# Optimization experiments

Measured on AMD Instinct MI355X. Metric: run time of the kernel, lower is better.

Reference implementation:

```python
import jax, jax.numpy as jnp
import numpy as np

EMBED_DIM = 1024
N_HEADS = 16
HEAD_DIM = EMBED_DIM // N_HEADS
N_CATS = 5
SCALE = float(np.sqrt(HEAD_DIM))


def setup_inputs() -> dict:
    key = jax.random.key(0)
    ks = jax.random.split(key, 16)
    B, S = 2, 2048
    inp = {
        "query": jax.random.normal(ks[0], (B, S, EMBED_DIM), jnp.float32),
        "key_": jax.random.normal(ks[1], (B, S, EMBED_DIM), jnp.float32),
        "value": jax.random.normal(ks[2], (B, S, EMBED_DIM), jnp.float32),
        "responses": jax.random.randint(ks[3], (B, S), 0, N_CATS),
        "mask": jnp.ones((B, S, S), jnp.int32),
        # Linear params (torch convention: y = x @ W.T + b)
        "Wq": jax.random.normal(ks[4], (EMBED_DIM, EMBED_DIM), jnp.float32) * 0.02,
        "bq": jnp.zeros((EMBED_DIM,), jnp.float32),
        "Wk": jax.random.normal(ks[5], (EMBED_DIM, EMBED_DIM), jnp.float32) * 0.02,
        "bk": jnp.zeros((EMBED_DIM,), jnp.float32),
        "Wv": jax.random.normal(ks[6], (EMBED_DIM, EMBED_DIM), jnp.float32) * 0.02,
        "bv": jnp.zeros((EMBED_DIM,), jnp.float32),
        "Wo": jax.random.normal(ks[7], (EMBED_DIM, EMBED_DIM), jnp.float32) * 0.02,
        "bo": jnp.zeros((EMBED_DIM,), jnp.float32),
        # qwk_modulation: Linear(1, n_heads)
        "Wm": jax.random.normal(ks[8], (N_HEADS, 1), jnp.float32) * 0.5,
        "bm": jnp.zeros((N_HEADS,), jnp.float32),
    }
    return inp


def _qwk_matrix():
    i = jnp.arange(N_CATS, dtype=jnp.float32)
    return 1.0 - (i[:, None] - i[None, :]) ** 2 / (N_CATS - 1) ** 2  # [C, C]


def reference(query, key_, value, responses, mask,
              Wq, bq, Wk, bk, Wv, bv, Wo, bo, Wm, bm):
    B, S, E = query.shape
    # projections
    Q = (query @ Wq.T + bq).reshape(B, S, N_HEADS, HEAD_DIM).transpose(0, 2, 1, 3)
    K = (key_ @ Wk.T + bk).reshape(B, S, N_HEADS, HEAD_DIM).transpose(0, 2, 1, 3)
    V = (value @ Wv.T + bv).reshape(B, S, N_HEADS, HEAD_DIM).transpose(0, 2, 1, 3)
    scores = jnp.einsum("bhqd,bhkd->bhqk", Q, K) / SCALE  # [B,H,S,S]
    # QWK ordinal bias: gather pairwise weight, tiny linear 1->H, broadcast-add
    qwk = _qwk_matrix()
    pair = qwk[responses[:, :, None], responses[:, None, :]]  # [B,S,S]
    # Linear(1, n_heads): bias[...,None] @ Wm.T + bm -> [B,S,S,H] -> [B,H,S,S]
    head_bias = pair[:, None, :, :] * Wm[:, 0][None, :, None, None] + bm[None, :, None, None]
    scores = scores + head_bias
    scores = jnp.where(mask[:, None, :, :] == 0, -1e9, scores)
    attn = jax.nn.softmax(scores, axis=-1)
    attended = jnp.einsum("bhqk,bhkd->bhqd", attn, V)
    attended = attended.transpose(0, 2, 1, 3).reshape(B, S, E)
    return attended @ Wo.T + bo
```

## Files before the change

### kernel.cpp

```cpp
#include <hip/hip_runtime.h>
#include <hip/hip_bf16.h>
#include <stdint.h>

#define S_LEN 2048
#define EMB   1024
#define NHEAD 16
#define HDIM  64
#define BATCH 2

typedef __bf16 bf16x8 __attribute__((ext_vector_type(8)));
typedef float  f32x4  __attribute__((ext_vector_type(4)));

__device__ __forceinline__ void gll16(const void* g, void* l) {
  __builtin_amdgcn_global_load_lds(
      (const __attribute__((address_space(1))) void*)g,
      (__attribute__((address_space(3))) void*)l,
      16, 0, 0);
}

__global__ void __launch_bounds__(256) cast_mask_kernel(
    const float* __restrict__ s0, const float* __restrict__ s1, const float* __restrict__ s2,
    const float* __restrict__ s3, const float* __restrict__ s4, const float* __restrict__ s5,
    const float* __restrict__ s6,
    __hip_bfloat16* __restrict__ d0, __hip_bfloat16* __restrict__ d1,
    __hip_bfloat16* __restrict__ d2, __hip_bfloat16* __restrict__ d3,
    __hip_bfloat16* __restrict__ d4, __hip_bfloat16* __restrict__ d5,
    __hip_bfloat16* __restrict__ d6,
    const int* __restrict__ mask, unsigned* __restrict__ flags) {
  const int z = blockIdx.y;
  const int t = threadIdx.x;
  if (z == 7) {
    const int kt = blockIdx.x & 15, qt = (blockIdx.x >> 4) & 31, b = (int)blockIdx.x >> 9;
    const int* base = mask + ((size_t)b * S_LEN + (size_t)qt * 64) * S_LEN + (size_t)kt * 128;
    int ok = 1;
#pragma unroll
    for (int p = 0; p < 8; ++p) {
      int idx = p * 256 + t;
      int row = idx >> 5, c4 = idx & 31;
      const int4 v = *(const int4*)(base + (size_t)row * S_LEN + c4 * 4);
      ok &= (v.x != 0) & (v.y != 0) & (v.z != 0) & (v.w != 0);
    }
    unsigned long long bl = __ballot(ok);
    __shared__ unsigned long long bw[4];
    bw[t >> 6] = bl;
    __syncthreads();
    if (t == 0) {
      unsigned all = ((bw[0] & bw[1] & bw[2] & bw[3]) == ~0ull) ? 1u : 0u;
      flags[((size_t)b * 32 + qt) * 16 + kt] = all;
    }
    return;
  }
  const float* s = (z == 0) ? s0 : (z == 1) ? s1 : (z == 2) ? s2 : (z == 3) ? s3
                 : (z == 4) ? s4 : (z == 5) ? s5 : s6;
  __hip_bfloat16* d = (z == 0) ? d0 : (z == 1) ? d1 : (z == 2) ? d2 : (z == 3) ? d3
                    : (z == 4) ? d4 : (z == 5) ? d5 : d6;
  const int n = (z < 3) ? (BATCH * S_LEN * EMB) : (EMB * EMB);
  const size_t i = ((size_t)blockIdx.x * 256 + t) * 16;
  if (i >= (size_t)n) return;
  __hip_bfloat16 tmp[16];
#pragma unroll
  for (int j = 0; j < 4; ++j) {
    const float4 v = *(const float4*)(s + i + j * 4);
    tmp[j * 4 + 0] = __float2bfloat16(v.x);
    tmp[j * 4 + 1] = __float2bfloat16(v.y);
    tmp[j * 4 + 2] = __float2bfloat16(v.z);
    tmp[j * 4 + 3] = __float2bfloat16(v.w);
  }
  *(bf16x8*)(d + i)     = *(bf16x8*)&tmp[0];
  *(bf16x8*)(d + i + 8) = *(bf16x8*)&tmp[8];
}

__global__ void __launch_bounds__(256, 2)
gemm_kernel(const __hip_bfloat16* __restrict__ A0, const __hip_bfloat16* __restrict__ A1,
            const __hip_bfloat16* __restrict__ A2,
            const __hip_bfloat16* __restrict__ W0, const __hip_bfloat16* __restrict__ W1,
            const __hip_bfloat16* __restrict__ W2,
            const float* __restrict__ b0, const float* __restrict__ b1,
            const float* __restrict__ b2,
            __hip_bfloat16* __restrict__ O0, __hip_bfloat16* __restrict__ O1,
            __hip_bfloat16* __restrict__ O2) {
  __shared__ __align__(16) __hip_bfloat16 As[128 * 64];
  __shared__ __align__(16) __hip_bfloat16 Bs[128 * 64];

  const int L = blockIdx.x;
  const int m0 = (L & 31) * 128;
  const int n0 = ((L >> 5) & 7) * 128;
  const int z  = L >> 8;

  const __hip_bfloat16* A  = (z == 0) ? A0 : ((z == 1) ? A1 : A2);
  const __hip_bfloat16* W  = (z == 0) ? W0 : ((z == 1) ? W1 : W2);
  const float* bi          = (z == 0) ? b0 : ((z == 1) ? b1 : b2);
  __hip_bfloat16* O        = (z == 0) ? O0 : ((z == 1) ? O1 : O2);

  const int t = threadIdx.x;
  const int w = t >> 6, lane = t & 63, quad = lane >> 4, l15 = lane & 15;
  const int wr = w >> 1, wc = w & 1;

  f32x4 acc[4][4];
#pragma unroll
  for (int i = 0; i < 4; ++i)
#pragma unroll
    for (int j = 0; j < 4; ++j) acc[i][j] = (f32x4)0.0f;

  const int srow = t >> 3;
  const int scb  = (t & 7) ^ (srow & 7);
  const __hip_bfloat16* Ap = A + (size_t)(m0 + srow) * EMB + (scb << 3);
  const __hip_bfloat16* Wp = W + (size_t)(n0 + srow) * EMB + (scb << 3);

  for (int k0 = 0; k0 < EMB; k0 += 64) {
    __syncthreads();
#pragma unroll
    for (int rnd = 0; rnd < 4; ++rnd) {
      gll16(Ap + (size_t)(rnd * 32) * EMB + k0, &As[(rnd * 256 + (w << 6)) * 8]);
      gll16(Wp + (size_t)(rnd * 32) * EMB + k0, &Bs[(rnd * 256 + (w << 6)) * 8]);
    }
    __syncthreads();

    bf16x8 af[4][2], bfr[4][2];
#pragma unroll
    for (int i = 0; i < 4; ++i) {
      const int ra = wr * 64 + i * 16 + l15;
#pragma unroll
      for (int hh = 0; hh < 2; ++hh)
        af[i][hh] = *(const bf16x8*)&As[ra * 64 + ((((hh << 2) + quad) ^ (l15 & 7)) << 3)];
    }
#pragma unroll
    for (int j = 0; j < 4; ++j) {
      const int rbw = wc * 64 + j * 16 + l15;
#pragma unroll
      for (int hh = 0; hh < 2; ++hh)
        bfr[j][hh] = *(const bf16x8*)&Bs[rbw * 64 + ((((hh << 2) + quad) ^ (l15 & 7)) << 3)];
    }
#pragma unroll
    for (int hh = 0; hh < 2; ++hh)
#pragma unroll
      for (int i = 0; i < 4; ++i)
#pragma unroll
        for (int j = 0; j < 4; ++j)
          acc[i][j] =
              __builtin_amdgcn_mfma_f32_16x16x32_bf16(af[i][hh], bfr[j][hh], acc[i][j], 0, 0, 0);
  }

#pragma unroll
  for (int j = 0; j < 4; ++j) {
    const int ng = n0 + wc * 64 + j * 16 + l15;
    const float bb = bi[ng];
    const int h = ng >> 6, d = ng & 63;
#pragma unroll
    for (int i = 0; i < 4; ++i) {
#pragma unroll
      for (int r = 0; r < 4; ++r) {
        const int mg = m0 + wr * 64 + i * 16 + quad * 4 + r;
        const int b = mg >> 11, s = mg & 2047;
        float v = acc[i][j][r] + bb;
        if (z == 0) {
          O[(((size_t)b * NHEAD + h) * S_LEN + s) * HDIM + d] =
              __float2bfloat16(v * (0.125f * 1.4426950408889634f));
        } else if (z == 1) {
          O[(((size_t)b * NHEAD + h) * S_LEN + s) * HDIM + d] = __float2bfloat16(v);
        } else {
          const size_t idx = (size_t)(b * NHEAD + h) * 131072 + (size_t)(s >> 7) * 8192 +
                             (size_t)((((s >> 5) & 3) * 4 + ((s >> 2) & 3)) * 64 + d) * 8 +
                             ((s >> 4) & 1) * 4 + (s & 3);
          O[idx] = __float2bfloat16(v);
        }
      }
    }
  }
}

__global__ void __launch_bounds__(256, 2)
gemm_o_kernel(const __hip_bfloat16* __restrict__ A, const __hip_bfloat16* __restrict__ W,
              const float* __restrict__ bi, float* __restrict__ O) {
  __shared__ __align__(16) __hip_bfloat16 As[64 * 64];
  __shared__ __align__(16) __hip_bfloat16 Bs[128 * 64];
  const int L = blockIdx.x;
  const int m0 = (L & 63) * 64;
  const int n0 = (L >> 6) * 128;
  const int t = threadIdx.x;
  const int w = t >> 6, lane = t & 63, quad = lane >> 4, l15 = lane & 15;
  const int wr = w >> 1, wc = w & 1;

  f32x4 acc[2][4];
#pragma unroll
  for (int i = 0; i < 2; ++i)
#pragma unroll
    for (int j = 0; j < 4; ++j) acc[i][j] = (f32x4)0.0f;

  const int srow = t >> 3;
  const int scb  = (t & 7) ^ (srow & 7);
  const __hip_bfloat16* Ap = A + (size_t)(m0 + srow) * EMB + (scb << 3);
  const __hip_bfloat16* Wp = W + (size_t)(n0 + srow) * EMB + (scb << 3);

  for (int k0 = 0; k0 < EMB; k0 += 64) {
    __syncthreads();
#pragma unroll
    for (int rnd = 0; rnd < 2; ++rnd)
      gll16(Ap + (size_t)(rnd * 32) * EMB + k0, &As[(rnd * 256 + (w << 6)) * 8]);
#pragma unroll
    for (int rnd = 0; rnd < 4; ++rnd)
      gll16(Wp + (size_t)(rnd * 32) * EMB + k0, &Bs[(rnd * 256 + (w << 6)) * 8]);
    __syncthreads();

    bf16x8 af[2][2], bfr[4][2];
#pragma unroll
    for (int i = 0; i < 2; ++i) {
      const int ra = wr * 32 + i * 16 + l15;
#pragma unroll
      for (int hh = 0; hh < 2; ++hh)
        af[i][hh] = *(const bf16x8*)&As[ra * 64 + ((((hh << 2) + quad) ^ (l15 & 7)) << 3)];
    }
#pragma unroll
    for (int j = 0; j < 4; ++j) {
      const int rbw = wc * 64 + j * 16 + l15;
#pragma unroll
      for (int hh = 0; hh < 2; ++hh)
        bfr[j][hh] = *(const bf16x8*)&Bs[rbw * 64 + ((((hh << 2) + quad) ^ (l15 & 7)) << 3)];
    }
#pragma unroll
    for (int hh = 0; hh < 2; ++hh)
#pragma unroll
      for (int i = 0; i < 2; ++i)
#pragma unroll
        for (int j = 0; j < 4; ++j)
          acc[i][j] =
              __builtin_amdgcn_mfma_f32_16x16x32_bf16(af[i][hh], bfr[j][hh], acc[i][j], 0, 0, 0);
  }

#pragma unroll
  for (int j = 0; j < 4; ++j) {
    const int ng = n0 + wc * 64 + j * 16 + l15;
    const float bb = bi[ng];
#pragma unroll
    for (int i = 0; i < 2; ++i) {
#pragma unroll
      for (int r = 0; r < 4; ++r) {
        const int mg = m0 + wr * 32 + i * 16 + quad * 4 + r;
        O[(size_t)mg * EMB + ng] = acc[i][j][r] + bb;
      }
    }
  }
}

__global__ void __launch_bounds__(512, 4)
flash_kernel(const __hip_bfloat16* __restrict__ qws, const __hip_bfloat16* __restrict__ kws,
             const __hip_bfloat16* __restrict__ vpk, const int* __restrict__ responses,
             const int* __restrict__ mask, const float* __restrict__ Wm,
             const unsigned* __restrict__ flags, __hip_bfloat16* __restrict__ att) {
  __shared__ __align__(16) unsigned char smem[32768];
  __shared__ unsigned char rb[S_LEN];
  __shared__ float lsm[512];

  __hip_bfloat16* Ks = (__hip_bfloat16*)smem;
  __hip_bfloat16* Vs = (__hip_bfloat16*)(smem + 16384);
  float* sm = (float*)smem;

  const int t = threadIdx.x;
  const int w = t >> 6, lane = t & 63, quad = lane >> 4, l15 = lane & 15;
  const int L = blockIdx.x;
  const int bh = L & 31;
  const int qt = L >> 5;
  const int b = bh >> 4, h = bh & 15;
  const int q0 = qt * 64;
  const int wq = w & 1, khalf = w >> 1;

#pragma unroll
  for (int i = 0; i < 4; ++i)
    rb[i * 512 + t] = (unsigned char)responses[b * S_LEN + i * 512 + t];

  const __hip_bfloat16* qbase = qws + ((size_t)bh * S_LEN + q0 + wq * 32) * HDIM;
  bf16x8 qf[2][2];
#pragma unroll
  for (int qg = 0; qg < 2; ++qg)
#pragma unroll
    for (int ks = 0; ks < 2; ++ks)
      qf[qg][ks] =
          *(const bf16x8*)(qbase + (size_t)(qg * 16 + l15) * HDIM + ks * 32 + quad * 8);

  const float c = Wm[h] * (0.0625f * 1.4426950408889634f);
  float A2[2];
#pragma unroll
  for (int qg = 0; qg < 2; ++qg)
    A2[qg] = 2.0f * c * (float)responses[b * S_LEN + q0 + wq * 32 + qg * 16 + l15];

  unsigned fmask;
  {
    const unsigned fv = flags[((size_t)b * 32 + qt) * 16 + (lane & 15)];
    fmask = (unsigned)__ballot(fv != 0u);
  }

  const __hip_bfloat16* kptr = kws + ((size_t)bh * S_LEN + (t >> 3)) * HDIM +
                               (((t & 7) ^ ((t >> 3) & 7)) << 3);
  const __hip_bfloat16* vptr = vpk + (size_t)bh * 131072 + (size_t)t * 8;

  float lsum[2] = {0.f, 0.f};
  f32x4 acc_o[2][4];
#pragma unroll
  for (int qg = 0; qg < 2; ++qg)
#pragma unroll
    for (int dt = 0; dt < 4; ++dt) acc_o[qg][dt] = (f32x4)0.0f;

  for (int kt = 0; kt < S_LEN / 128; ++kt) {
    __syncthreads();
#pragma unroll
    for (int p = 0; p < 2; ++p) {
      gll16(kptr + p * 64 * HDIM, &Ks[(p * 512 + (w << 6)) * 8]);
      gll16(vptr + p * 4096,      &Vs[(p * 512 + (w << 6)) * 8]);
    }
    kptr += 128 * HDIM;
    vptr += 8192;
    __syncthreads();

    const bool fl = (fmask >> kt) & 1u;

    bf16x8 pfr[2];
#pragma unroll
    for (int ct = 0; ct < 2; ++ct) {
      const int rowk = khalf * 32 + ct * 16 + l15;
      bf16x8 kf0 = *(const bf16x8*)&Ks[rowk * 64 + ((quad ^ (l15 & 7)) << 3)];
      bf16x8 kf1 = *(const bf16x8*)&Ks[rowk * 64 + (((4 + quad) ^ (l15 & 7)) << 3)];
      const unsigned ru = *(const unsigned*)&rb[kt * 128 + khalf * 32 + ct * 16 + quad * 4];
#pragma unroll
      for (int qg = 0; qg < 2; ++qg) {
        f32x4 sc = __builtin_amdgcn_mfma_f32_16x16x32_bf16(kf0, qf[qg][0], (f32x4)0.0f, 0, 0, 0);
        sc = __builtin_amdgcn_mfma_f32_16x16x32_bf16(kf1, qf[qg][1], sc, 0, 0, 0);
        __hip_bfloat16 pb[4];
#pragma unroll
        for (int r = 0; r < 4; ++r) {
          const float rkf = (float)((ru >> (8 * r)) & 255u);
          const float sb = fmaf(rkf, fmaf(-c, rkf, A2[qg]), sc[r]);
          float p = __builtin_amdgcn_exp2f(sb);
          if (!fl) {
            int mq = mask[((size_t)b * S_LEN + q0 + wq * 32 + qg * 16 + l15) * S_LEN +
                          kt * 128 + khalf * 32 + ct * 16 + quad * 4 + r];
            p = mq ? p : 0.0f;
          }
          lsum[qg] += p;
          pb[r] = __float2bfloat16(p);
        }
        __hip_bfloat16* half = (__hip_bfloat16*)&pfr[qg] + ct * 4;
        half[0] = pb[0]; half[1] = pb[1]; half[2] = pb[2]; half[3] = pb[3];
      }
    }

#pragma unroll
    for (int dt = 0; dt < 4; ++dt) {
      bf16x8 vv = *(const bf16x8*)&Vs[(((khalf << 2) + quad) * 64 + (dt << 4) + l15) << 3];
#pragma unroll
      for (int qg = 0; qg < 2; ++qg)
        acc_o[qg][dt] =
            __builtin_amdgcn_mfma_f32_16x16x32_bf16(pfr[qg], vv, acc_o[qg][dt], 0, 0, 0);
    }
  }

  __syncthreads();
  if (khalf & 1) {
    float* dst = sm + (khalf >> 1) * 4096;
#pragma unroll
    for (int qg = 0; qg < 2; ++qg) {
#pragma unroll
      for (int dt = 0; dt < 4; ++dt)
        *(f32x4*)&dst[(((wq * 2 + qg) * 4) + dt) * 256 + lane * 4] = acc_o[qg][dt];
      lsm[(khalf >> 1) * 256 + (wq * 2 + qg) * 64 + lane] = lsum[qg];
    }
  }
  __syncthreads();
  if (!(khalf & 1)) {
    const float* src = sm + (khalf >> 1) * 4096;
#pragma unroll
    for (int qg = 0; qg < 2; ++qg) {
#pragma unroll
      for (int dt = 0; dt < 4; ++dt)
        acc_o[qg][dt] += *(const f32x4*)&src[(((wq * 2 + qg) * 4) + dt) * 256 + lane * 4];
      lsum[qg] += lsm[(khalf >> 1) * 256 + (wq * 2 + qg) * 64 + lane];
    }
  }
  if (khalf == 2) {
    float* dst = sm + 4096;
#pragma unroll
    for (int qg = 0; qg < 2; ++qg) {
#pragma unroll
      for (int dt = 0; dt < 4; ++dt)
        *(f32x4*)&dst[(((wq * 2 + qg) * 4) + dt) * 256 + lane * 4] = acc_o[qg][dt];
      lsm[256 + (wq * 2 + qg) * 64 + lane] = lsum[qg];
    }
  }
  __syncthreads();
  if (khalf == 0) {
    const float* src = sm + 4096;
#pragma unroll
    for (int qg = 0; qg < 2; ++qg) {
#pragma unroll
      for (int dt = 0; dt < 4; ++dt)
        acc_o[qg][dt] += *(const f32x4*)&src[(((wq * 2 + qg) * 4) + dt) * 256 + lane * 4];
      lsum[qg] += lsm[256 + (wq * 2 + qg) * 64 + lane];
      lsum[qg] += __shfl_xor(lsum[qg], 16, 64);
      lsum[qg] += __shfl_xor(lsum[qg], 32, 64);
      float inv[4];
#pragma unroll
      for (int r = 0; r < 4; ++r) inv[r] = 1.0f / __shfl(lsum[qg], quad * 4 + r, 64);
#pragma unroll
      for (int dt = 0; dt < 4; ++dt)
#pragma unroll
        for (int r = 0; r < 4; ++r)
          att[((size_t)b * S_LEN + q0 + wq * 32 + qg * 16 + quad * 4 + r) * EMB +
              h * HDIM + dt * 16 + l15] = __float2bfloat16(acc_o[qg][dt][r] * inv[r]);
    }
  }
}

extern "C" void kernel_launch(void* const* d_in, const int* in_sizes, int n_in,
                              void* d_out, int out_size, void* d_ws, size_t ws_size,
                              hipStream_t stream) {
  const float* query = (const float*)d_in[0];
  const float* key_  = (const float*)d_in[1];
  const float* value = (const float*)d_in[2];
  const int* responses = (const int*)d_in[3];
  const int* mask      = (const int*)d_in[4];
  const float* Wq = (const float*)d_in[5];
  const float* bq = (const float*)d_in[6];
  const float* Wk = (const float*)d_in[7];
  const float* bk = (const float*)d_in[8];
  const float* Wv = (const float*)d_in[9];
  const float* bv = (const float*)d_in[10];
  const float* Wo = (const float*)d_in[11];
  const float* bo = (const float*)d_in[12];
  const float* Wm = (const float*)d_in[13];

  __hip_bfloat16* ws = (__hip_bfloat16*)d_ws;
  const size_t NTOK = (size_t)BATCH * S_LEN * EMB;
  const size_t NW   = (size_t)EMB * EMB;
  __hip_bfloat16* qcast = ws;
  __hip_bfloat16* kcast = ws + NTOK;
  __hip_bfloat16* vcast = ws + 2 * NTOK;
  __hip_bfloat16* wqb   = ws + 3 * NTOK;
  __hip_bfloat16* wkb   = wqb + NW;
  __hip_bfloat16* wvb   = wqb + 2 * NW;
  __hip_bfloat16* wob   = wqb + 3 * NW;
  __hip_bfloat16* qws   = wqb + 4 * NW;
  __hip_bfloat16* kws   = qws + NTOK;
  __hip_bfloat16* vpk   = qws + 2 * NTOK;
  __hip_bfloat16* att   = qws + 3 * NTOK;
  unsigned* flags       = (unsigned*)(qws + 4 * NTOK);
  float* out            = (float*)d_out;

  cast_mask_kernel<<<dim3(1024, 8), 256, 0, stream>>>(
      query, key_, value, Wq, Wk, Wv, Wo,
      qcast, kcast, vcast, wqb, wkb, wvb, wob, mask, flags);
  gemm_kernel<<<768, 256, 0, stream>>>(qcast, kcast, vcast, wqb, wkb, wvb,
                                       bq, bk, bv, qws, kws, vpk);
  flash_kernel<<<1024, 512, 0, stream>>>(qws, kws, vpk, responses, mask,
                                         Wm, flags, att);
  gemm_o_kernel<<<512, 256, 0, stream>>>(att, wob, bo, out);
}
```

Baseline: 254.4 us.

## Load K/V fragments directly from global memory instead of LDS staging

The flash kernel no longer stages each 128-row K/V tile into shared memory with global_load_lds. Each wave now reads its own K and V MFMA fragments straight from global memory into registers. This drops the two block-wide barriers per key tile and lets waves proceed independently. The cost is that K and V fragments are fetched redundantly across the two query-half waves and rely on cache hits, and K reads lose the swizzled LDS layout.

```diff
diff --git a/kernel.cpp b/kernel.cpp
--- a/kernel.cpp
+++ b/kernel.cpp
@@ -251,8 +251,6 @@
   __shared__ unsigned char rb[S_LEN];
   __shared__ float lsm[512];
 
-  __hip_bfloat16* Ks = (__hip_bfloat16*)smem;
-  __hip_bfloat16* Vs = (__hip_bfloat16*)(smem + 16384);
   float* sm = (float*)smem;
 
   const int t = threadIdx.x;
@@ -289,9 +287,8 @@
     fmask = (unsigned)__ballot(fv != 0u);
   }
 
-  const __hip_bfloat16* kptr = kws + ((size_t)bh * S_LEN + (t >> 3)) * HDIM +
-                               (((t & 7) ^ ((t >> 3) & 7)) << 3);
-  const __hip_bfloat16* vptr = vpk + (size_t)bh * 131072 + (size_t)t * 8;
+  const __hip_bfloat16* kb = kws + (size_t)bh * S_LEN * HDIM;
+  const __hip_bfloat16* vb = vpk + (size_t)bh * 131072;
 
   float lsum[2] = {0.f, 0.f};
   f32x4 acc_o[2][4];
@@ -300,30 +297,34 @@
 #pragma unroll
     for (int dt = 0; dt < 4; ++dt) acc_o[qg][dt] = (f32x4)0.0f;
 
+  __syncthreads();
+
   for (int kt = 0; kt < S_LEN / 128; ++kt) {
-    __syncthreads();
-#pragma unroll
-    for (int p = 0; p < 2; ++p) {
-      gll16(kptr + p * 64 * HDIM, &Ks[(p * 512 + (w << 6)) * 8]);
-      gll16(vptr + p * 4096,      &Vs[(p * 512 + (w << 6)) * 8]);
-    }
-    kptr += 128 * HDIM;
-    vptr += 8192;
-    __syncthreads();
-
     const bool fl = (fmask >> kt) & 1u;
 
+    bf16x8 kf[2][2];
+#pragma unroll
+    for (int ct = 0; ct < 2; ++ct) {
+      const __hip_bfloat16* kr =
+          kb + (size_t)(kt * 128 + khalf * 32 + ct * 16 + l15) * HDIM + quad * 8;
+      kf[ct][0] = *(const bf16x8*)(kr);
+      kf[ct][1] = *(const bf16x8*)(kr + 32);
+    }
+    bf16x8 vv[4];
+#pragma unroll
+    for (int dt = 0; dt < 4; ++dt)
+      vv[dt] = *(const bf16x8*)(vb + (size_t)kt * 8192 +
+               ((((khalf << 2) + quad) * 64 + (dt << 4) + l15) << 3));
+
     bf16x8 pfr[2];
 #pragma unroll
     for (int ct = 0; ct < 2; ++ct) {
-      const int rowk = khalf * 32 + ct * 16 + l15;
-      bf16x8 kf0 = *(const bf16x8*)&Ks[rowk * 64 + ((quad ^ (l15 & 7)) << 3)];
-      bf16x8 kf1 = *(const bf16x8*)&Ks[rowk * 64 + (((4 + quad) ^ (l15 & 7)) << 3)];
       const unsigned ru = *(const unsigned*)&rb[kt * 128 + khalf * 32 + ct * 16 + quad * 4];
 #pragma unroll
       for (int qg = 0; qg < 2; ++qg) {
-        f32x4 sc = __builtin_amdgcn_mfma_f32_16x16x32_bf16(kf0, qf[qg][0], (f32x4)0.0f, 0, 0, 0);
-        sc = __builtin_amdgcn_mfma_f32_16x16x32_bf16(kf1, qf[qg][1], sc, 0, 0, 0);
+        f32x4 sc =
+            __builtin_amdgcn_mfma_f32_16x16x32_bf16(kf[ct][0], qf[qg][0], (f32x4)0.0f, 0, 0, 0);
+        sc = __builtin_amdgcn_mfma_f32_16x16x32_bf16(kf[ct][1], qf[qg][1], sc, 0, 0, 0);
         __hip_bfloat16 pb[4];
 #pragma unroll
         for (int r = 0; r < 4; ++r) {
@@ -345,15 +346,13 @@
 
 #pragma unroll
     for (int dt = 0; dt < 4; ++dt) {
-      bf16x8 vv = *(const bf16x8*)&Vs[(((khalf << 2) + quad) * 64 + (dt << 4) + l15) << 3];
 #pragma unroll
       for (int qg = 0; qg < 2; ++qg)
         acc_o[qg][dt] =
-            __builtin_amdgcn_mfma_f32_16x16x32_bf16(pfr[qg], vv, acc_o[qg][dt], 0, 0, 0);
-    }
-  }
-
-  __syncthreads();
+            __builtin_amdgcn_mfma_f32_16x16x32_bf16(pfr[qg], vv[dt], acc_o[qg][dt], 0, 0, 0);
+    }
+  }
+
   if (khalf & 1) {
     float* dst = sm + (khalf >> 1) * 4096;
 #pragma unroll
```

Result: slower. 287.6 us (+13.0%).
